# Optimization experiments

Hardware: AMD Instinct MI355X
Metric: run time of the kernel (lower is better)

Reference implementation:

```python
import jax, jax.numpy as jnp
import numpy as np

N, D = 320, 256
TEMP = 2.0

# case ids sorted: [-11,-10,-1,0,1,10,11]; value order: [0,1,2,3,11,12,13]
CASE_VALS = jnp.array([-11, -10, -1, 0, 1, 10, 11], dtype=jnp.int32)
TABLE = jnp.array([
    [0, 2, 2, 1, 1, 0, 1],   # case -11
    [0, 2, 2, 2, 2, 2, 2],   # case -10
    [0, 2, 2, 2, 1, 0, 2],   # case -1
    [0, 2, 2, 2, 2, 2, 2],   # case 0
    [0, 2, 2, 2, 1, 2, 2],   # case 1
    [0, 2, 2, 2, 2, 0, 2],   # case 10
    [0, 2, 2, 1, 1, 0, 1],   # case 11
], dtype=jnp.int32)


def setup_inputs() -> dict:
    key = jax.random.key(0)
    k1, k2, k3 = jax.random.split(key, 3)
    features = jax.random.normal(k1, (N, D), dtype=jnp.float32)
    y_times = jax.random.uniform(k2, (N,), dtype=jnp.float32)
    y_events = jax.random.randint(k3, (N,), 0, 2, dtype=jnp.int32)
    return {"features": features, "y_times": y_times, "y_events": y_events}


def _forward(features, y_times, y_events):
    n = features.shape[0]
    # pairwise -L2 similarity / temperature  (safe sqrt: diag is 0)
    diff = features[:, None, :] - features[None, :, :]          # [N,N,D]
    d2 = jnp.sum(diff * diff, axis=-1)                           # [N,N]
    norm = jnp.where(d2 > 0, jnp.sqrt(jnp.where(d2 > 0, d2, 1.0)), 0.0)
    logits = -norm / TEMP
    logits = logits - jax.lax.stop_gradient(jnp.max(logits, axis=1, keepdims=True))
    exp_logits = jnp.exp(logits)

    idx = jnp.arange(n)
    eye = idx[:, None] == idx[None, :]

    def per_anchor(k):
        pld = y_times - y_times[k]                               # [N]
        abs_i = jnp.abs(pld)[:, None]                            # |pld[i]|
        pj = pld[None, :]                                        # pld[j]
        # sequential torch mask assignments collapse to this piecewise map
        td = jnp.where(pj > abs_i, 3,
             jnp.where(-pj > abs_i, 1,
             jnp.where(jnp.abs(pj) > 0, 2, 0))).astype(jnp.int32)
        td = jnp.where(eye, 0, td)                               # fill_diagonal_(0)
        neg = jnp.where(td != 0, y_events[None, :] * 10 + td, 0) # {0,1,2,3,11,12,13}
        sgn = jnp.sign(pld).astype(jnp.int32)
        cid = (y_events + 10 * y_events[k]) * sgn                # per-row case id
        cidx = jnp.searchsorted(CASE_VALS, cid)                  # [N]
        vidx = jnp.where(neg > 3, neg - 7, neg)                  # map vals to 0..6
        mapped = TABLE[cidx[:, None], vidx]                      # numba lookup, fused
        final = (mapped == 1).astype(jnp.float32) + 0.5 * (mapped == 2)
        keep = (idx != k).astype(jnp.float32)                    # delete row/col k
        final = final * keep[:, None] * keep[None, :]
        valid = jnp.sum(final, axis=-1) > 0                      # [N]
        Np = jnp.sum(valid)
        denom = jnp.sum(final * exp_logits, axis=-1)             # masked sum-exp
        logp = logits[:, k] - jnp.log(jnp.where(valid, denom, 1.0))
        loss_k = -jnp.sum(jnp.where(valid, logp, 0.0)) / jnp.maximum(Np, 1)
        return jnp.where(Np > 0, loss_k, 0.0), (Np > 0)

    losses, has_pos = jax.vmap(per_anchor)(idx)
    return jnp.sum(losses) / jnp.sum(has_pos)


def reference(features, y_times, y_events):
    return _forward(features, y_times, y_events)
```

## Files before the change

kernel.cpp:

```cpp
#include <hip/hip_runtime.h>
#include <math.h>

#define NN 320
#define DD 256
#define PS 328

__device__ __constant__ unsigned int c_PACK[7] =
    {0x2294u, 0x1554u, 0x1254u, 0x1554u, 0x1654u, 0x1154u, 0x2294u};

__global__ __launch_bounds__(256) void prep_kernel(
    const float* __restrict__ F, const float* __restrict__ yt,
    const int* __restrict__ ye, float4* __restrict__ FT4,
    float4* __restrict__ meta) {
    __shared__ float sh[64 * 65];
    const int b = blockIdx.x;
    if (b < 20) {
        float (*tile)[65] = (float(*)[65])sh;
        const int I = b % 5;
        const int J = b / 5;
        const int lane = threadIdx.x & 63;
        const int quad = threadIdx.x >> 6;
#pragma unroll
        for (int r0 = 0; r0 < 64; r0 += 4) {
            const int r = r0 + quad;
            tile[r][lane] = F[(I * 64 + r) * DD + J * 64 + lane];
        }
        __syncthreads();
#pragma unroll
        for (int q = 0; q < 16; q += 4) {
            const int d4 = q + quad;
            float4 v = make_float4(tile[lane][d4 * 4 + 0], tile[lane][d4 * 4 + 1],
                                   tile[lane][d4 * 4 + 2], tile[lane][d4 * 4 + 3]);
            FT4[(J * 16 + d4) * NN + I * 64 + lane] = v;
        }
    } else {
        float* s_t = sh;
        for (int j = threadIdx.x; j < NN; j += 256) s_t[j] = yt[j];
        __syncthreads();
        for (int j = threadIdx.x; j < NN; j += 256) {
            const float tj = s_t[j];
            int lt = 0, le = 0, pos = 0;
            for (int l = 0; l < NN; ++l) {
                const float tl = s_t[l];
                lt  += (tl < tj);
                le  += (tl <= tj);
                pos += (tl < tj) || (tl == tj && l < j);
            }
            meta[j] = make_float4(tj, __int_as_float(lt), __int_as_float(le),
                                  __int_as_float(pos | (ye[j] << 16)));
        }
    }
}

__global__ __launch_bounds__(NN) void pair_scan_kernel(
    const float* __restrict__ F, const float4* __restrict__ FT4,
    const float4* __restrict__ meta, float* __restrict__ L,
    float* __restrict__ P0, float* __restrict__ P1) {
    __shared__ __align__(16) float fi[DD];
    __shared__ float A0[2][NN];
    __shared__ float A1[2][NN];
    const int i = blockIdx.x;
    const int j = threadIdx.x;
    if (j < DD) fi[j] = F[i * DD + j];
    __syncthreads();

    const float4* __restrict__ fi4 = (const float4*)fi;
    float a0 = 0.f, a1 = 0.f, a2 = 0.f, a3 = 0.f;
#pragma unroll 8
    for (int d4 = 0; d4 < DD / 4; ++d4) {
        const float4 f4 = fi4[d4];
        const float4 g4 = FT4[d4 * NN + j];
        const float u0 = f4.x - g4.x, u1 = f4.y - g4.y;
        const float u2 = f4.z - g4.z, u3 = f4.w - g4.w;
        a0 = fmaf(u0, u0, a0);
        a1 = fmaf(u1, u1, a1);
        a2 = fmaf(u2, u2, a2);
        a3 = fmaf(u3, u3, a3);
    }
    const float d2 = (a0 + a1) + (a2 + a3);
    const float nrm = (d2 > 0.f) ? sqrtf(d2) : 0.f;
    const float lg = -0.5f * nrm;
    L[i * NN + j] = lg;
    const float e = expf(lg);

    const int pe  = __float_as_int(meta[j].w);
    const int pos = pe & 0xFFFF;
    const int ev  = pe >> 16;
    A0[0][pos] = ev ? 0.f : e;
    A1[0][pos] = ev ? e : 0.f;
    __syncthreads();

    int src = 0;
#pragma unroll
    for (int off = 1; off < NN; off <<= 1) {
        const int dst = src ^ 1;
        float v0 = A0[src][j], v1 = A1[src][j];
        if (j >= off) { v0 += A0[src][j - off]; v1 += A1[src][j - off]; }
        A0[dst][j] = v0;
        A1[dst][j] = v1;
        __syncthreads();
        src = dst;
    }

    P0[i * PS + j] = (j == 0) ? 0.f : A0[src][j - 1];
    P1[i * PS + j] = (j == 0) ? 0.f : A1[src][j - 1];
    if (j == NN - 1) {
        P0[i * PS + NN] = A0[src][j];
        P1[i * PS + NN] = A1[src][j];
    }
}

__global__ __launch_bounds__(NN) void anchor_kernel(
    const float4* __restrict__ meta, const float* __restrict__ L,
    const float* __restrict__ P0, const float* __restrict__ P1,
    float* __restrict__ accv) {
    __shared__ float swl[5];
    __shared__ float swn[5];
    const int k = blockIdx.x;
    const int i = threadIdx.x;
    const int wave = i >> 6, lane = i & 63;

    const float4 mk = meta[k];
    const float4 mi = meta[i];
    const float tk = mk.x, ti = mi.x;
    const int rlt_k = __float_as_int(mk.y), rle_k = __float_as_int(mk.z);
    const int evk   = __float_as_int(mk.w) >> 16;
    const int rlt_i = __float_as_int(mi.y), rle_i = __float_as_int(mi.z);
    const int evi   = __float_as_int(mi.w) >> 16;

    const int sgn = (ti > tk) ? 1 : ((ti < tk) ? -1 : 0);
    const unsigned pack = c_PACK[3 + sgn * (evi + 2 * evk)];
    const int rlo = min(rlt_i, rlt_k);
    const int rhi = max(rle_i, rle_k);

    const float* __restrict__ b0 = P0 + i * PS;
    const float* __restrict__ b1 = P1 + i * PS;
    const float q0lo = b0[rlo], q0hi = b0[rhi], q0a = b0[rlt_k], q0b = b0[rle_k], t0 = b0[NN];
    const float q1lo = b1[rlo], q1hi = b1[rhi], q1a = b1[rlt_k], q1b = b1[rle_k], t1 = b1[NN];

    const float LO0 = q0lo, HI0 = t0 - q0hi, MI0 = q0hi - q0lo - (q0b - q0a);
    const float LO1 = q1lo, HI1 = t1 - q1hi, MI1 = q1hi - q1lo - (q1b - q1a);

    const float c1 = (float)((pack >> 2) & 3u),  c2 = (float)((pack >> 4) & 3u);
    const float c3 = (float)((pack >> 6) & 3u),  c4 = (float)((pack >> 8) & 3u);
    const float c5 = (float)((pack >> 10) & 3u), c6 = (float)((pack >> 12) & 3u);

    float dx = c1 * LO0 + c2 * MI0 + c3 * HI0 + c4 * LO1 + c5 * MI1 + c6 * HI1;
    if (ti != tk) dx -= (float)((pack >> (2 * (2 + 3 * evi))) & 3u);

    float lp = 0.f, np = 0.f;
    if (i != k && dx > 0.f) {
        lp = L[k * NN + i] - logf(0.5f * dx);
        np = 1.f;
    }
#pragma unroll
    for (int off = 32; off > 0; off >>= 1) {
        lp += __shfl_down(lp, off);
        np += __shfl_down(np, off);
    }
    if (lane == 0) { swl[wave] = lp; swn[wave] = np; }
    __syncthreads();
    if (i == 0) {
        float s = 0.f, n = 0.f;
#pragma unroll
        for (int w = 0; w < 5; ++w) { s += swl[w]; n += swn[w]; }
        accv[k] = s;
        accv[NN + k] = n;
    }
}

__global__ __launch_bounds__(NN) void finalize_kernel(
    const float* __restrict__ accv, float* __restrict__ out) {
    __shared__ float s_l[5];
    __shared__ float s_h[5];
    const int k = threadIdx.x;
    const int wave = k >> 6, lane = k & 63;
    const float np = accv[NN + k];
    float loss = (np > 0.f) ? (-accv[k] / np) : 0.f;
    float has  = (np > 0.f) ? 1.f : 0.f;
#pragma unroll
    for (int off = 32; off > 0; off >>= 1) {
        loss += __shfl_down(loss, off);
        has  += __shfl_down(has, off);
    }
    if (lane == 0) { s_l[wave] = loss; s_h[wave] = has; }
    __syncthreads();
    if (k == 0) {
        float tl = 0.f, th = 0.f;
#pragma unroll
        for (int w = 0; w < 5; ++w) { tl += s_l[w]; th += s_h[w]; }
        out[0] = tl / th;
    }
}

extern "C" void kernel_launch(void* const* d_in, const int* in_sizes, int n_in,
                              void* d_out, int out_size, void* d_ws, size_t ws_size,
                              hipStream_t stream) {
    const float* F  = (const float*)d_in[0];
    const float* yt = (const float*)d_in[1];
    const int*   ye = (const int*)d_in[2];
    float* out = (float*)d_out;
    float* ws  = (float*)d_ws;

    float4* meta = (float4*)ws;
    float4* FT4  = (float4*)(ws + 4 * NN);
    float*  L    = ws + 4 * NN + 4 * (DD / 4) * NN;
    float*  P0   = L + NN * NN;
    float*  P1   = P0 + NN * PS;
    float*  accv = P1 + NN * PS;

    prep_kernel<<<21, 256, 0, stream>>>(F, yt, ye, FT4, meta);
    pair_scan_kernel<<<NN, NN, 0, stream>>>(F, FT4, meta, L, P0, P1);
    anchor_kernel<<<NN, NN, 0, stream>>>(meta, L, P0, P1, accv);
    finalize_kernel<<<1, NN, 0, stream>>>(accv, out);
}
```

Baseline: 94.59 us.

## Use wave-shuffle scan in double precision and fuse finalize via atomics

Replaces the shared-memory Hillis-Steele prefix scan, which needed nine block barriers, with a 64-lane shuffle scan plus a per-wave offset pass, and carries the prefix sums in double precision. The diagonal term is now zeroed at scan time, so the per-element subtraction in the anchor kernel goes away. The separate finalize launch is folded into the anchor kernel through atomic accumulation and a last-block ticket. The cost is double the scan buffer traffic, slower FP64 arithmetic, and atomic contention, and the float atomic sums become order-dependent.

```diff
diff --git a/kernel.cpp b/kernel.cpp
--- a/kernel.cpp
+++ b/kernel.cpp
@@ -11,7 +11,7 @@
 __global__ __launch_bounds__(256) void prep_kernel(
     const float* __restrict__ F, const float* __restrict__ yt,
     const int* __restrict__ ye, float4* __restrict__ FT4,
-    float4* __restrict__ meta) {
+    float4* __restrict__ meta, float* __restrict__ acc) {
     __shared__ float sh[64 * 65];
     const int b = blockIdx.x;
     if (b < 20) {
@@ -34,6 +34,7 @@
             FT4[(J * 16 + d4) * NN + I * 64 + lane] = v;
         }
     } else {
+        if (threadIdx.x < 4) acc[threadIdx.x] = 0.0f;
         float* s_t = sh;
         for (int j = threadIdx.x; j < NN; j += 256) s_t[j] = yt[j];
         __syncthreads();
@@ -55,12 +56,15 @@
 __global__ __launch_bounds__(NN) void pair_scan_kernel(
     const float* __restrict__ F, const float4* __restrict__ FT4,
     const float4* __restrict__ meta, float* __restrict__ L,
-    float* __restrict__ P0, float* __restrict__ P1) {
+    double* __restrict__ P0, double* __restrict__ P1) {
     __shared__ __align__(16) float fi[DD];
-    __shared__ float A0[2][NN];
-    __shared__ float A1[2][NN];
+    __shared__ double sA0[NN];
+    __shared__ double sA1[NN];
+    __shared__ double sW0[5];
+    __shared__ double sW1[5];
     const int i = blockIdx.x;
     const int j = threadIdx.x;
+    const int wave = j >> 6, lane = j & 63;
     if (j < DD) fi[j] = F[i * DD + j];
     __syncthreads();
 
@@ -83,37 +87,39 @@
     L[i * NN + j] = lg;
     const float e = expf(lg);
 
-    const int pe  = __float_as_int(meta[j].w);
-    const int pos = pe & 0xFFFF;
-    const int ev  = pe >> 16;
-    A0[0][pos] = ev ? 0.f : e;
-    A1[0][pos] = ev ? e : 0.f;
-    __syncthreads();
-
-    int src = 0;
-#pragma unroll
-    for (int off = 1; off < NN; off <<= 1) {
-        const int dst = src ^ 1;
-        float v0 = A0[src][j], v1 = A1[src][j];
-        if (j >= off) { v0 += A0[src][j - off]; v1 += A1[src][j - off]; }
-        A0[dst][j] = v0;
-        A1[dst][j] = v1;
-        __syncthreads();
-        src = dst;
-    }
-
-    P0[i * PS + j] = (j == 0) ? 0.f : A0[src][j - 1];
-    P1[i * PS + j] = (j == 0) ? 0.f : A1[src][j - 1];
+    const int pw  = __float_as_int(meta[j].w);
+    const int pos = pw & 0xFFFF;
+    const int ev  = pw >> 16;
+    const double ed = (j == i) ? 0.0 : (double)e;
+    sA0[pos] = ev ? 0.0 : ed;
+    sA1[pos] = ev ? ed : 0.0;
+    __syncthreads();
+
+    const double v0 = sA0[j], v1 = sA1[j];
+    double inc0 = v0, inc1 = v1;
+#pragma unroll
+    for (int off = 1; off < 64; off <<= 1) {
+        const double u0 = __shfl_up(inc0, off);
+        const double u1 = __shfl_up(inc1, off);
+        if (lane >= off) { inc0 += u0; inc1 += u1; }
+    }
+    if (lane == 63) { sW0[wave] = inc0; sW1[wave] = inc1; }
+    __syncthreads();
+    double o0 = 0.0, o1 = 0.0;
+    for (int w = 0; w < wave; ++w) { o0 += sW0[w]; o1 += sW1[w]; }
+
+    P0[i * PS + j] = inc0 + o0 - v0;
+    P1[i * PS + j] = inc1 + o1 - v1;
     if (j == NN - 1) {
-        P0[i * PS + NN] = A0[src][j];
-        P1[i * PS + NN] = A1[src][j];
-    }
-}
-
-__global__ __launch_bounds__(NN) void anchor_kernel(
+        P0[i * PS + NN] = inc0 + o0;
+        P1[i * PS + NN] = inc1 + o1;
+    }
+}
+
+__global__ __launch_bounds__(NN) void anchor_final_kernel(
     const float4* __restrict__ meta, const float* __restrict__ L,
-    const float* __restrict__ P0, const float* __restrict__ P1,
-    float* __restrict__ accv) {
+    const double* __restrict__ P0, const double* __restrict__ P1,
+    float* __restrict__ acc, float* __restrict__ out) {
     __shared__ float swl[5];
     __shared__ float swn[5];
     const int k = blockIdx.x;
@@ -133,24 +139,24 @@
     const int rlo = min(rlt_i, rlt_k);
     const int rhi = max(rle_i, rle_k);
 
-    const float* __restrict__ b0 = P0 + i * PS;
-    const float* __restrict__ b1 = P1 + i * PS;
-    const float q0lo = b0[rlo], q0hi = b0[rhi], q0a = b0[rlt_k], q0b = b0[rle_k], t0 = b0[NN];
-    const float q1lo = b1[rlo], q1hi = b1[rhi], q1a = b1[rlt_k], q1b = b1[rle_k], t1 = b1[NN];
-
-    const float LO0 = q0lo, HI0 = t0 - q0hi, MI0 = q0hi - q0lo - (q0b - q0a);
-    const float LO1 = q1lo, HI1 = t1 - q1hi, MI1 = q1hi - q1lo - (q1b - q1a);
-
-    const float c1 = (float)((pack >> 2) & 3u),  c2 = (float)((pack >> 4) & 3u);
-    const float c3 = (float)((pack >> 6) & 3u),  c4 = (float)((pack >> 8) & 3u);
-    const float c5 = (float)((pack >> 10) & 3u), c6 = (float)((pack >> 12) & 3u);
-
-    float dx = c1 * LO0 + c2 * MI0 + c3 * HI0 + c4 * LO1 + c5 * MI1 + c6 * HI1;
-    if (ti != tk) dx -= (float)((pack >> (2 * (2 + 3 * evi))) & 3u);
+    const double* __restrict__ b0 = P0 + i * PS;
+    const double* __restrict__ b1 = P1 + i * PS;
+    const double q0lo = b0[rlo], q0hi = b0[rhi], q0a = b0[rlt_k], q0b = b0[rle_k], t0 = b0[NN];
+    const double q1lo = b1[rlo], q1hi = b1[rhi], q1a = b1[rlt_k], q1b = b1[rle_k], t1 = b1[NN];
+
+    const double LO0 = q0lo, HI0 = t0 - q0hi, MI0 = q0hi - q0lo - (q0b - q0a);
+    const double LO1 = q1lo, HI1 = t1 - q1hi, MI1 = q1hi - q1lo - (q1b - q1a);
+
+    const double c1 = (double)((pack >> 2) & 3u),  c2 = (double)((pack >> 4) & 3u);
+    const double c3 = (double)((pack >> 6) & 3u),  c4 = (double)((pack >> 8) & 3u);
+    const double c5 = (double)((pack >> 10) & 3u), c6 = (double)((pack >> 12) & 3u);
+
+    const double dx = c1 * LO0 + c2 * MI0 + c3 * HI0
+                    + c4 * LO1 + c5 * MI1 + c6 * HI1;
 
     float lp = 0.f, np = 0.f;
-    if (i != k && dx > 0.f) {
-        lp = L[k * NN + i] - logf(0.5f * dx);
+    if (i != k && dx > 0.0) {
+        lp = L[k * NN + i] - logf((float)(0.5 * dx));
         np = 1.f;
     }
 #pragma unroll
@@ -164,32 +170,17 @@
         float s = 0.f, n = 0.f;
 #pragma unroll
         for (int w = 0; w < 5; ++w) { s += swl[w]; n += swn[w]; }
-        accv[k] = s;
-        accv[NN + k] = n;
-    }
-}
-
-__global__ __launch_bounds__(NN) void finalize_kernel(
-    const float* __restrict__ accv, float* __restrict__ out) {
-    __shared__ float s_l[5];
-    __shared__ float s_h[5];
-    const int k = threadIdx.x;
-    const int wave = k >> 6, lane = k & 63;
-    const float np = accv[NN + k];
-    float loss = (np > 0.f) ? (-accv[k] / np) : 0.f;
-    float has  = (np > 0.f) ? 1.f : 0.f;
-#pragma unroll
-    for (int off = 32; off > 0; off >>= 1) {
-        loss += __shfl_down(loss, off);
-        has  += __shfl_down(has, off);
-    }
-    if (lane == 0) { s_l[wave] = loss; s_h[wave] = has; }
-    __syncthreads();
-    if (k == 0) {
-        float tl = 0.f, th = 0.f;
-#pragma unroll
-        for (int w = 0; w < 5; ++w) { tl += s_l[w]; th += s_h[w]; }
-        out[0] = tl / th;
+        if (n > 0.f) {
+            atomicAdd(&acc[0], -(s / n));
+            atomicAdd(&acc[1], 1.0f);
+        }
+        __threadfence();
+        const unsigned tkt = atomicAdd((unsigned int*)(acc + 2), 1u);
+        if (tkt == NN - 1) {
+            const float ls = atomicAdd(&acc[0], 0.0f);
+            const float hs = atomicAdd(&acc[1], 0.0f);
+            out[0] = ls / hs;
+        }
     }
 }
 
@@ -205,12 +196,11 @@
     float4* meta = (float4*)ws;
     float4* FT4  = (float4*)(ws + 4 * NN);
     float*  L    = ws + 4 * NN + 4 * (DD / 4) * NN;
-    float*  P0   = L + NN * NN;
-    float*  P1   = P0 + NN * PS;
-    float*  accv = P1 + NN * PS;
-
-    prep_kernel<<<21, 256, 0, stream>>>(F, yt, ye, FT4, meta);
+    float*  acc  = L + NN * NN;
+    double* P0   = (double*)(acc + 4);
+    double* P1   = P0 + NN * PS;
+
+    prep_kernel<<<21, 256, 0, stream>>>(F, yt, ye, FT4, meta, acc);
     pair_scan_kernel<<<NN, NN, 0, stream>>>(F, FT4, meta, L, P0, P1);
-    anchor_kernel<<<NN, NN, 0, stream>>>(meta, L, P0, P1, accv);
-    finalize_kernel<<<1, NN, 0, stream>>>(accv, out);
-}
+    anchor_final_kernel<<<NN, NN, 0, stream>>>(meta, L, P0, P1, acc, out);
+}
```

Result: slower. 105.4 us (+11.4%).
